# Kernel tuning notes

Measured on AMD Instinct MI355X. Metric: run time of the kernel, lower is better.

Reference implementation:

```python
import jax, jax.numpy as jnp
import numpy as np
from jax import lax

DN = ('NCHW', 'OIHW', 'NCHW')


def conv_reflect(x, w, b, pad):
    # reflect-padded Conv2d (padding_mode='reflect' in torch)
    xp = jnp.pad(x, ((0, 0), (0, 0), (pad, pad), (pad, pad)), mode='reflect')
    y = lax.conv_general_dilated(xp, w, (1, 1), 'VALID', dimension_numbers=DN)
    return y + b[None, :, None, None]


def setup_inputs() -> dict:
    key = jax.random.key(0)
    ks = jax.random.split(key, 11)
    B, C_in, W, H = 2, 20, 1024, 1024
    K = 16          # num_preconv_kernls
    P = 9           # preconv_kernel_size
    hid = 8         # hidden_input_size
    s = 0.05
    x = jax.random.normal(ks[0], (B, C_in, W, H), dtype=jnp.float32)
    w1 = jax.random.normal(ks[1], (16, 20, 7, 7), dtype=jnp.float32) * s
    b1 = jnp.zeros((16,), jnp.float32)
    w2 = jax.random.normal(ks[2], (32, 16, 5, 5), dtype=jnp.float32) * s
    b2 = jnp.zeros((32,), jnp.float32)
    w3 = jax.random.normal(ks[3], (64, 32, 5, 5), dtype=jnp.float32) * s
    b3 = jnp.zeros((64,), jnp.float32)
    w4 = jax.random.normal(ks[4], (hid + K, 64, 5, 5), dtype=jnp.float32) * s
    b4 = jnp.zeros((hid + K,), jnp.float32)
    dwk = (jnp.ones((K, 1, P, P), jnp.float32)
           + jax.random.normal(ks[5], (K, 1, P, P), dtype=jnp.float32) * 0.1) / (P * P)
    return {"x": x, "w1": w1, "b1": b1, "w2": w2, "b2": b2,
            "w3": w3, "b3": b3, "w4": w4, "b4": b4, "dwk": dwk}


def reference(x, w1, b1, w2, b2, w3, b3, w4, b4, dwk):
    B, _, W, H = x.shape
    hid, K, P = 8, 16, 9
    color = x[:, 0:3]                                   # (B,3,W,H)
    h = jax.nn.relu(conv_reflect(x, w1, b1, 3))
    h = jax.nn.relu(conv_reflect(h, w2, b2, 2))
    h = jax.nn.relu(conv_reflect(h, w3, b3, 2))
    raw = conv_reflect(h, w4, b4, 2)                    # (B,24,W,H)
    hidden = raw[:, 0:hid]                              # (B,8,W,H)
    weights = jax.nn.softmax(raw[:, hid:] / 5.0, axis=1)  # (B,16,W,H)
    # depthwise conv of color with 16 kernels per channel (groups=3, zero pad)
    rpk = jnp.tile(dwk, (3, 1, 1, 1))                   # (48,1,P,P)
    pre = lax.conv_general_dilated(color, rpk, (1, 1),
                                   [(P // 2, P // 2), (P // 2, P // 2)],
                                   dimension_numbers=DN,
                                   feature_group_count=3)
    pre = pre.reshape(B, 3, K, W, H)
    filtered = jnp.einsum('bkwh,bckwh->bcwh', weights, pre)
    return jnp.concatenate((filtered, hidden), axis=1)  # (B,11,W,H)
```

## Files before the change

kernel.cpp:

```cpp
#include <hip/hip_runtime.h>

constexpr int IMG = 1024;
constexpr long long HW = (long long)IMG * IMG;

typedef unsigned short u16;
typedef __attribute__((ext_vector_type(8))) short bf16x8;
typedef __attribute__((ext_vector_type(4))) float f32x4;
typedef __attribute__((ext_vector_type(4))) u16 u16x4;

__device__ __forceinline__ int reflect_idx(int i, int n) {
    if (i < 0) i = -i;
    if (i >= n) i = 2 * n - 2 - i;
    return i;
}
__device__ __forceinline__ int iclamp(int v, int lo, int hi) {
    return v < lo ? lo : (v > hi ? hi : v);
}
__device__ __forceinline__ u16 f2bf(float f) {
    unsigned u = __builtin_bit_cast(unsigned, f);
    u += 0x7FFF + ((u >> 16) & 1);
    return (u16)(u >> 16);
}

__global__ void prep_w1(const float* __restrict__ w1, u16* __restrict__ w1p) {
    int i = blockIdx.x * 256 + threadIdx.x;
    if (i >= 49 * 16 * 32) return;
    int tap = i / (16 * 32), rem = i % (16 * 32), co = rem / 32, ci = rem % 32;
    w1p[i] = (ci < 20) ? f2bf(w1[(co * 20 + ci) * 49 + tap]) : (u16)0;
}
__global__ void prep_w2(const float* __restrict__ w2, u16* __restrict__ w2p) {
    int i = blockIdx.x * 256 + threadIdx.x;
    if (i >= 13 * 32 * 32) return;
    int p = i / (32 * 32), rem = i % (32 * 32), co = rem / 32, k = rem % 32;
    int tap = 2 * p + (k >> 4), ci = k & 15;
    w2p[i] = (tap < 25) ? f2bf(w2[(co * 16 + ci) * 25 + tap]) : (u16)0;
}
__global__ void prep_w3(const float* __restrict__ w3, u16* __restrict__ w3p) {
    int i = blockIdx.x * 256 + threadIdx.x;
    if (i >= 25 * 64 * 32) return;
    int tap = i / (64 * 32), rem = i % (64 * 32), co = rem / 32, ci = rem % 32;
    w3p[i] = f2bf(w3[(co * 32 + ci) * 25 + tap]);
}
__global__ void prep_w4(const float* __restrict__ w4, u16* __restrict__ w4p) {
    int i = blockIdx.x * 256 + threadIdx.x;
    if (i >= 25 * 32 * 64) return;
    int tap = i / (32 * 64), rem = i % (32 * 64), co = rem / 64, ci = rem % 64;
    w4p[i] = (co < 24) ? f2bf(w4[(co * 64 + ci) * 25 + tap]) : (u16)0;
}

__global__ __launch_bounds__(256) void conv1_mfma(
    const float* __restrict__ x, const u16* __restrict__ w1p,
    const float* __restrict__ b1, u16* __restrict__ h1,
    int out_base, int out_rows)
{
    constexpr int TS = 22, PAD = 3, UNITS = 4;
    __shared__ u16 tile[TS * TS * 32];

    const int tid = threadIdx.x;
    const int gx0 = blockIdx.x * 16;
    const int gy0 = out_base + blockIdx.y * 16;

    for (int u = tid; u < TS * TS * UNITS; u += 256) {
        int pu = u >> 2, q = u & 3;
        int ty = pu / TS, tx = pu - ty * TS;
        int gy = reflect_idx(gy0 + ty - PAD, IMG);
        int gx = reflect_idx(gx0 + tx - PAD, IMG);
        long long off = (long long)gy * IMG + gx;
        bf16x8 v;
        #pragma unroll
        for (int j = 0; j < 8; ++j) {
            int cc = q * 8 + j;
            float f = (cc < 20) ? x[(long long)cc * HW + off] : 0.f;
            v[j] = (short)f2bf(f);
        }
        *(bf16x8*)&tile[(pu * UNITS + (q ^ (tx & 3))) * 8] = v;
    }
    __syncthreads();

    const int lane = tid & 63, wv = tid >> 6;
    const int l15 = lane & 15, g = lane >> 4;

    f32x4 acc[4];
    #pragma unroll
    for (int y = 0; y < 4; ++y) acc[y] = (f32x4){0.f, 0.f, 0.f, 0.f};

    for (int dx = 0; dx < 7; ++dx) {
        bf16x8 af[7];
        #pragma unroll
        for (int dy = 0; dy < 7; ++dy)
            af[dy] = *(const bf16x8*)&w1p[((dy * 7 + dx) * 16 + l15) * 32 + g * 8];
        bf16x8 bfr[10];
        const int tx = l15 + dx;
        #pragma unroll
        for (int r = 0; r < 10; ++r)
            bfr[r] = *(const bf16x8*)&tile[(((wv * 4 + r) * TS + tx) * UNITS + (g ^ (tx & 3))) * 8];
        #pragma unroll
        for (int yy = 0; yy < 4; ++yy)
            #pragma unroll
            for (int dy = 0; dy < 7; ++dy)
                acc[yy] = __builtin_amdgcn_mfma_f32_16x16x32_bf16(af[dy], bfr[yy + dy], acc[yy], 0, 0, 0);
    }

    const int out_hi = out_base + out_rows;
    float bia[4];
    #pragma unroll
    for (int r = 0; r < 4; ++r) bia[r] = b1[4 * g + r];
    #pragma unroll
    for (int yy = 0; yy < 4; ++yy) {
        int gy = gy0 + wv * 4 + yy;
        if (gy >= out_hi) continue;
        u16x4 pk;
        #pragma unroll
        for (int r = 0; r < 4; ++r)
            pk[r] = f2bf(fmaxf(acc[yy][r] + bia[r], 0.f));
        *(u16x4*)&h1[((long long)(gy - out_base) * IMG + gx0 + l15) * 16 + 4 * g] = pk;
    }
}

__global__ __launch_bounds__(256) void conv2_mfma(
    const u16* __restrict__ h1, const u16* __restrict__ w2p,
    const float* __restrict__ b2, u16* __restrict__ h2,
    int in_base, int in_rows, int out_base, int out_rows)
{
    constexpr int TS = 20, PAD = 2, UNITS = 2;
    __shared__ u16 tile[TS * TS * 16];

    const int tid = threadIdx.x;
    const int gx0 = blockIdx.x * 16;
    const int gy0 = out_base + blockIdx.y * 16;

    for (int u = tid; u < TS * TS * UNITS; u += 256) {
        int pu = u >> 1, q = u & 1;
        int ty = pu / TS, tx = pu - ty * TS;
        int gy = reflect_idx(gy0 + ty - PAD, IMG) - in_base;
        gy = iclamp(gy, 0, in_rows - 1);
        int gx = reflect_idx(gx0 + tx - PAD, IMG);
        bf16x8 v = *(const bf16x8*)&h1[((long long)gy * IMG + gx) * 16 + q * 8];
        *(bf16x8*)&tile[(pu * UNITS + (q ^ (tx & 1))) * 8] = v;
    }
    __syncthreads();

    const int lane = tid & 63, wv = tid >> 6;
    const int l15 = lane & 15, g = lane >> 4;

    f32x4 acc[4][2];
    #pragma unroll
    for (int y = 0; y < 4; ++y) {
        acc[y][0] = (f32x4){0.f, 0.f, 0.f, 0.f};
        acc[y][1] = (f32x4){0.f, 0.f, 0.f, 0.f};
    }

    for (int p = 0; p < 13; ++p) {
        int tap = 2 * p + (g >> 1);
        int tb = tap > 24 ? 24 : tap;
        int dy = tb / 5, dx = tb - dy * 5;
        bf16x8 af0 = *(const bf16x8*)&w2p[(p * 32 + l15) * 32 + g * 8];
        bf16x8 af1 = *(const bf16x8*)&w2p[(p * 32 + 16 + l15) * 32 + g * 8];
        const int tx = l15 + dx;
        #pragma unroll
        for (int yy = 0; yy < 4; ++yy) {
            int ty = wv * 4 + yy + dy;
            bf16x8 bf = *(const bf16x8*)&tile[((ty * TS + tx) * UNITS + ((g & 1) ^ (tx & 1))) * 8];
            acc[yy][0] = __builtin_amdgcn_mfma_f32_16x16x32_bf16(af0, bf, acc[yy][0], 0, 0, 0);
            acc[yy][1] = __builtin_amdgcn_mfma_f32_16x16x32_bf16(af1, bf, acc[yy][1], 0, 0, 0);
        }
    }

    const int out_hi = out_base + out_rows;
    #pragma unroll
    for (int yy = 0; yy < 4; ++yy) {
        int gy = gy0 + wv * 4 + yy;
        if (gy >= out_hi) continue;
        long long pb = ((long long)(gy - out_base) * IMG + gx0 + l15) * 32;
        #pragma unroll
        for (int cb = 0; cb < 2; ++cb) {
            int co = cb * 16 + 4 * g;
            u16x4 pk;
            #pragma unroll
            for (int r = 0; r < 4; ++r)
                pk[r] = f2bf(fmaxf(acc[yy][cb][r] + b2[co + r], 0.f));
            *(u16x4*)&h2[pb + co] = pk;
        }
    }
}

__global__ __launch_bounds__(256) void conv3_mfma(
    const u16* __restrict__ h2, const u16* __restrict__ w3p,
    const float* __restrict__ b3, u16* __restrict__ h3,
    int in_base, int in_rows, int out_base, int out_rows)
{
    constexpr int CI = 32, TS = 20, PAD = 2, UNITS = 4;
    __shared__ u16 tile[TS * TS * CI];

    const int tid = threadIdx.x;
    const int gx0 = blockIdx.x * 16;
    const int gy0 = out_base + blockIdx.y * 16;

    for (int u = tid; u < TS * TS * UNITS; u += 256) {
        int pu = u >> 2, q = u & 3;
        int ty = pu / TS, tx = pu - ty * TS;
        int gy = reflect_idx(gy0 + ty - PAD, IMG) - in_base;
        gy = iclamp(gy, 0, in_rows - 1);
        int gx = reflect_idx(gx0 + tx - PAD, IMG);
        bf16x8 v = *(const bf16x8*)&h2[((long long)gy * IMG + gx) * CI + q * 8];
        *(bf16x8*)&tile[(pu * UNITS + (q ^ (tx & 3))) * 8] = v;
    }
    __syncthreads();

    const int lane = tid & 63, wv = tid >> 6;
    const int l15 = lane & 15, g = lane >> 4;

    f32x4 acc[4][4];
    #pragma unroll
    for (int y = 0; y < 4; ++y)
        #pragma unroll
        for (int cb = 0; cb < 4; ++cb) acc[y][cb] = (f32x4){0.f, 0.f, 0.f, 0.f};

    for (int dx = 0; dx < 5; ++dx) {
        const int tx = l15 + dx;
        const int uu = g ^ (tx & 3);
        bf16x8 bfr[8];
        #pragma unroll
        for (int s = 0; s < 8; ++s)
            bfr[s] = *(const bf16x8*)&tile[(((wv * 4 + s) * TS + tx) * UNITS + uu) * 8];
        #pragma unroll
        for (int dy = 0; dy < 5; ++dy) {
            const int tap = dy * 5 + dx;
            bf16x8 af[4];
            #pragma unroll
            for (int cb = 0; cb < 4; ++cb)
                af[cb] = *(const bf16x8*)&w3p[(tap * 64 + cb * 16 + l15) * 32 + g * 8];
            #pragma unroll
            for (int yy = 0; yy < 4; ++yy)
                #pragma unroll
                for (int cb = 0; cb < 4; ++cb)
                    acc[yy][cb] = __builtin_amdgcn_mfma_f32_16x16x32_bf16(af[cb], bfr[yy + dy], acc[yy][cb], 0, 0, 0);
        }
    }

    const int out_hi = out_base + out_rows;
    #pragma unroll
    for (int yy = 0; yy < 4; ++yy) {
        int gy = gy0 + wv * 4 + yy;
        if (gy >= out_hi) continue;
        long long pb = ((long long)(gy - out_base) * IMG + gx0 + l15) * 64;
        #pragma unroll
        for (int cb = 0; cb < 4; ++cb) {
            int co = cb * 16 + 4 * g;
            u16x4 pk;
            #pragma unroll
            for (int r = 0; r < 4; ++r)
                pk[r] = f2bf(fmaxf(acc[yy][cb][r] + b3[co + r], 0.f));
            *(u16x4*)&h3[pb + co] = pk;
        }
    }
}

__global__ __launch_bounds__(256) void conv4_mfma(
    const u16* __restrict__ h3, const u16* __restrict__ w4p,
    const float* __restrict__ b4, float* __restrict__ out,
    float* __restrict__ wsoft, int in_base, int in_rows, int row0, int nrows)
{
    constexpr int CI = 64, TS = 20, PAD = 2, UNITS = 4;
    __shared__ u16 tile[TS * TS * 32];

    const int tid = threadIdx.x;
    const int gx0 = blockIdx.x * 16;
    const int gy0 = row0 + blockIdx.y * 16;

    const int lane = tid & 63, wv = tid >> 6;
    const int l15 = lane & 15, g = lane >> 4;

    f32x4 acc[4][2];
    #pragma unroll
    for (int y = 0; y < 4; ++y) {
        acc[y][0] = (f32x4){0.f, 0.f, 0.f, 0.f};
        acc[y][1] = (f32x4){0.f, 0.f, 0.f, 0.f};
    }

    #pragma unroll
    for (int half = 0; half < 2; ++half) {
        if (half) __syncthreads();
        for (int u = tid; u < TS * TS * UNITS; u += 256) {
            int pu = u >> 2, q = u & 3;
            int ty = pu / TS, tx = pu - ty * TS;
            int gy = reflect_idx(gy0 + ty - PAD, IMG) - in_base;
            gy = iclamp(gy, 0, in_rows - 1);
            int gx = reflect_idx(gx0 + tx - PAD, IMG);
            bf16x8 v = *(const bf16x8*)&h3[((long long)gy * IMG + gx) * CI + half * 32 + q * 8];
            *(bf16x8*)&tile[(pu * UNITS + (q ^ (tx & 3))) * 8] = v;
        }
        __syncthreads();

        for (int dx = 0; dx < 5; ++dx) {
            const int tx = l15 + dx;
            const int uu = g ^ (tx & 3);
            bf16x8 bfr[8];
            #pragma unroll
            for (int s = 0; s < 8; ++s)
                bfr[s] = *(const bf16x8*)&tile[(((wv * 4 + s) * TS + tx) * UNITS + uu) * 8];
            #pragma unroll
            for (int dy = 0; dy < 5; ++dy) {
                const int tap = dy * 5 + dx;
                bf16x8 af0 = *(const bf16x8*)&w4p[(tap * 32 + l15) * 64 + half * 32 + g * 8];
                bf16x8 af1 = *(const bf16x8*)&w4p[(tap * 32 + 16 + l15) * 64 + half * 32 + g * 8];
                #pragma unroll
                for (int yy = 0; yy < 4; ++yy) {
                    acc[yy][0] = __builtin_amdgcn_mfma_f32_16x16x32_bf16(af0, bfr[yy + dy], acc[yy][0], 0, 0, 0);
                    acc[yy][1] = __builtin_amdgcn_mfma_f32_16x16x32_bf16(af1, bfr[yy + dy], acc[yy][1], 0, 0, 0);
                }
            }
        }
    }

    float bia0[4], bia1[4];
    #pragma unroll
    for (int r = 0; r < 4; ++r) {
        bia0[r] = b4[4 * g + r];
        int c1 = 16 + 4 * g + r;
        bia1[r] = (c1 < 24) ? b4[c1] : 0.f;
    }

    #pragma unroll
    for (int yy = 0; yy < 4; ++yy) {
        int gy = gy0 + wv * 4 + yy;
        long long pg = (long long)gy * IMG + gx0 + l15;
        float v0[4], v1[4];
        #pragma unroll
        for (int r = 0; r < 4; ++r) {
            v0[r] = acc[yy][0][r] + bia0[r];
            v1[r] = acc[yy][1][r] + bia1[r];
        }
        if (g < 2) {
            #pragma unroll
            for (int r = 0; r < 4; ++r)
                out[(long long)(3 + 4 * g + r) * HW + pg] = v0[r];
        }
        float s[4];
        int kbase;
        if (g < 2) {
            kbase = 8 + 4 * g;
            #pragma unroll
            for (int r = 0; r < 4; ++r) s[r] = v1[r] * 0.2f;
        } else {
            kbase = 4 * (g - 2);
            #pragma unroll
            for (int r = 0; r < 4; ++r) s[r] = v0[r] * 0.2f;
        }
        float m = fmaxf(fmaxf(s[0], s[1]), fmaxf(s[2], s[3]));
        m = fmaxf(m, __shfl_xor(m, 16));
        m = fmaxf(m, __shfl_xor(m, 32));
        float e[4], loc = 0.f;
        #pragma unroll
        for (int r = 0; r < 4; ++r) { e[r] = __expf(s[r] - m); loc += e[r]; }
        loc += __shfl_xor(loc, 16);
        loc += __shfl_xor(loc, 32);
        float inv = 1.f / loc;
        long long pl = (long long)(gy - row0) * IMG + gx0 + l15;
        #pragma unroll
        for (int r = 0; r < 4; ++r)
            wsoft[(long long)(kbase + r) * nrows * IMG + pl] = e[r] * inv;
    }
}

__global__ __launch_bounds__(256) void apply_filter(
    const float* __restrict__ x, const float* __restrict__ dwk,
    const float* __restrict__ wsoft, float* __restrict__ out,
    int row0, int nrows)
{
    constexpr int PAD = 4, TSF = 40;
    __shared__ float ctile[3][TSF * TSF];

    const int tid = threadIdx.x;
    const int tx = tid & 7, ty = tid >> 3;
    const int bx = blockIdx.x * 32;
    const int gy0 = row0 + blockIdx.y * 32;

    for (int c = 0; c < 3; ++c)
        for (int idx = tid; idx < TSF * TSF; idx += 256) {
            int ly = idx / TSF, lx = idx - ly * TSF;
            int gy = gy0 + ly - PAD, gx = bx + lx - PAD;
            float v = 0.f;
            if (gy >= 0 && gy < IMG && gx >= 0 && gx < IMG)
                v = x[(long long)c * HW + (long long)gy * IMG + gx];
            ctile[c][idx] = v;
        }
    __syncthreads();

    const int gy = gy0 + ty;
    const int xq = bx + tx * 4;

    float wreg[16][4];
    #pragma unroll
    for (int k = 0; k < 16; ++k) {
        f32x4 wv4 = *(const f32x4*)&wsoft[((long long)k * nrows + (gy - row0)) * IMG + xq];
        #pragma unroll
        for (int p = 0; p < 4; ++p) wreg[k][p] = wv4[p];
    }

    float f[3][4];
    #pragma unroll
    for (int c = 0; c < 3; ++c)
        #pragma unroll
        for (int p = 0; p < 4; ++p) f[c][p] = 0.f;

    for (int dy = 0; dy < 9; ++dy) {
        float c9[9][4];
        #pragma unroll
        for (int dxx = 0; dxx < 9; ++dxx)
            #pragma unroll
            for (int p = 0; p < 4; ++p) c9[dxx][p] = 0.f;
        #pragma unroll
        for (int k = 0; k < 16; ++k) {
            #pragma unroll
            for (int dxx = 0; dxx < 9; ++dxx) {
                float s = dwk[k * 81 + dy * 9 + dxx];
                #pragma unroll
                for (int p = 0; p < 4; ++p) c9[dxx][p] += s * wreg[k][p];
            }
        }
        #pragma unroll
        for (int c = 0; c < 3; ++c) {
            const float* crow = &ctile[c][(ty + dy) * TSF + tx * 4];
            f32x4 q0 = *(const f32x4*)crow;
            f32x4 q1 = *(const f32x4*)(crow + 4);
            f32x4 q2 = *(const f32x4*)(crow + 8);
            float win[12];
            #pragma unroll
            for (int j = 0; j < 4; ++j) { win[j] = q0[j]; win[4 + j] = q1[j]; win[8 + j] = q2[j]; }
            #pragma unroll
            for (int dxx = 0; dxx < 9; ++dxx)
                #pragma unroll
                for (int p = 0; p < 4; ++p)
                    f[c][p] += c9[dxx][p] * win[dxx + p];
        }
    }

    #pragma unroll
    for (int c = 0; c < 3; ++c) {
        f32x4 o = { f[c][0], f[c][1], f[c][2], f[c][3] };
        *(f32x4*)&out[(long long)c * HW + (long long)gy * IMG + xq] = o;
    }
}

static inline int hmax(int a, int b) { return a > b ? a : b; }
static inline int hmin(int a, int b) { return a < b ? a : b; }

extern "C" void kernel_launch(void* const* d_in, const int* in_sizes, int n_in,
                              void* d_out, int out_size, void* d_ws, size_t ws_size,
                              hipStream_t stream) {
    const float* x   = (const float*)d_in[0];
    const float* w1  = (const float*)d_in[1];
    const float* b1  = (const float*)d_in[2];
    const float* w2  = (const float*)d_in[3];
    const float* b2  = (const float*)d_in[4];
    const float* w3  = (const float*)d_in[5];
    const float* b3  = (const float*)d_in[6];
    const float* w4  = (const float*)d_in[7];
    const float* b4  = (const float*)d_in[8];
    const float* dwk = (const float*)d_in[9];
    float* out = (float*)d_out;

    int R = 32;
    const int cand[6] = {1024, 512, 256, 128, 64, 32};
    for (int i = 0; i < 6; ++i) {
        long long r = cand[i];
        size_t need = 32768ULL * (r + 12) + 65536ULL * (r + 8)
                    + 131072ULL * (r + 4) + 65536ULL * r + 400000ULL;
        if (need <= ws_size) { R = cand[i]; break; }
    }

    u16*   h1    = (u16*)d_ws;
    u16*   h2    = h1 + (long long)(R + 12) * IMG * 16;
    u16*   h3    = h2 + (long long)(R + 8) * IMG * 32;
    float* wsoft = (float*)(h3 + (long long)(R + 4) * IMG * 64);
    u16*   w1p   = (u16*)(wsoft + 16LL * R * IMG);
    u16*   w2p   = w1p + 49 * 16 * 32;
    u16*   w3p   = w2p + 13 * 32 * 32;
    u16*   w4p   = w3p + 25 * 64 * 32;

    dim3 blk(256);
    prep_w1<<<dim3(98),  blk, 0, stream>>>(w1, w1p);
    prep_w2<<<dim3(52),  blk, 0, stream>>>(w2, w2p);
    prep_w3<<<dim3(200), blk, 0, stream>>>(w3, w3p);
    prep_w4<<<dim3(200), blk, 0, stream>>>(w4, w4p);

    const int nstripes = IMG / R;
    for (int b = 0; b < 2; ++b) {
        const float* x_b = x + (long long)b * 20 * HW;
        float* out_b = out + (long long)b * 11 * HW;
        for (int s = 0; s < nstripes; ++s) {
            const int r0 = s * R;
            const int h1_lo = hmax(0, r0 - 6), h1_hi = hmin(IMG, r0 + R + 6), h1_r = h1_hi - h1_lo;
            const int h2_lo = hmax(0, r0 - 4), h2_hi = hmin(IMG, r0 + R + 4), h2_r = h2_hi - h2_lo;
            const int h3_lo = hmax(0, r0 - 2), h3_hi = hmin(IMG, r0 + R + 2), h3_r = h3_hi - h3_lo;

            conv1_mfma<<<dim3(64, (h1_r + 15) / 16, 1), blk, 0, stream>>>(
                x_b, w1p, b1, h1, h1_lo, h1_r);
            conv2_mfma<<<dim3(64, (h2_r + 15) / 16, 1), blk, 0, stream>>>(
                h1, w2p, b2, h2, h1_lo, h1_r, h2_lo, h2_r);
            conv3_mfma<<<dim3(64, (h3_r + 15) / 16, 1), blk, 0, stream>>>(
                h2, w3p, b3, h3, h2_lo, h2_r, h3_lo, h3_r);
            conv4_mfma<<<dim3(64, R / 16, 1), blk, 0, stream>>>(
                h3, w4p, b4, out_b, wsoft, h3_lo, h3_r, r0, R);
            apply_filter<<<dim3(32, R / 32, 1), blk, 0, stream>>>(
                x_b, dwk, wsoft, out_b, r0, R);
        }
    }
}
```

Baseline: 1.204 ms.

## Stage conv3/conv4 input tiles via direct global-to-LDS loads and double-buffer conv4 halves

Replaces register-staged tile fills in conv3 and conv4 with __builtin_amdgcn_global_load_lds direct-to-LDS 16-byte loads. The swizzle moves from the LDS destination to the global source address, because each wave writes a contiguous 1 KiB LDS chunk. conv4 now uses two LDS tiles and issues the second-half load before computing on the first, so the load can overlap with MFMA work. This doubles conv4's LDS footprint, which may lower occupancy. Correctness depends on the direct-LDS load semantics and on the __syncthreads placement making the data visible.

```diff
diff --git a/kernel.cpp b/kernel.cpp
--- a/kernel.cpp
+++ b/kernel.cpp
@@ -195,20 +195,22 @@
     const int tid = threadIdx.x;
     const int gx0 = blockIdx.x * 16;
     const int gy0 = out_base + blockIdx.y * 16;
-
-    for (int u = tid; u < TS * TS * UNITS; u += 256) {
-        int pu = u >> 2, q = u & 3;
-        int ty = pu / TS, tx = pu - ty * TS;
-        int gy = reflect_idx(gy0 + ty - PAD, IMG) - in_base;
-        gy = iclamp(gy, 0, in_rows - 1);
-        int gx = reflect_idx(gx0 + tx - PAD, IMG);
-        bf16x8 v = *(const bf16x8*)&h2[((long long)gy * IMG + gx) * CI + q * 8];
-        *(bf16x8*)&tile[(pu * UNITS + (q ^ (tx & 3))) * 8] = v;
-    }
-    __syncthreads();
-
     const int lane = tid & 63, wv = tid >> 6;
     const int l15 = lane & 15, g = lane >> 4;
+
+    for (int gidx = wv; gidx < 25; gidx += 4) {
+        int j = (gidx << 6) + lane;
+        int pu = j >> 2, qq = j & 3;
+        int ty = pu / TS, tx = pu - ty * TS;
+        int gy = iclamp(reflect_idx(gy0 + ty - PAD, IMG) - in_base, 0, in_rows - 1);
+        int gx = reflect_idx(gx0 + tx - PAD, IMG);
+        const u16* src = &h2[((long long)gy * IMG + gx) * CI + ((qq ^ (tx & 3)) << 3)];
+        __builtin_amdgcn_global_load_lds(
+            (const __attribute__((address_space(1))) void*)src,
+            (__attribute__((address_space(3))) void*)&tile[(long long)gidx << 9],
+            16, 0, 0);
+    }
+    __syncthreads();
 
     f32x4 acc[4][4];
     #pragma unroll
@@ -262,14 +264,29 @@
     float* __restrict__ wsoft, int in_base, int in_rows, int row0, int nrows)
 {
     constexpr int CI = 64, TS = 20, PAD = 2, UNITS = 4;
-    __shared__ u16 tile[TS * TS * 32];
+    __shared__ u16 tileA[TS * TS * 32];
+    __shared__ u16 tileB[TS * TS * 32];
 
     const int tid = threadIdx.x;
     const int gx0 = blockIdx.x * 16;
     const int gy0 = row0 + blockIdx.y * 16;
-
     const int lane = tid & 63, wv = tid >> 6;
     const int l15 = lane & 15, g = lane >> 4;
+
+    auto STAGE = [&](u16* tl, int half) {
+        for (int gidx = wv; gidx < 25; gidx += 4) {
+            int j = (gidx << 6) + lane;
+            int pu = j >> 2, qq = j & 3;
+            int ty = pu / TS, tx = pu - ty * TS;
+            int gy = iclamp(reflect_idx(gy0 + ty - PAD, IMG) - in_base, 0, in_rows - 1);
+            int gx = reflect_idx(gx0 + tx - PAD, IMG);
+            const u16* src = &h3[((long long)gy * IMG + gx) * CI + half * 32 + ((qq ^ (tx & 3)) << 3)];
+            __builtin_amdgcn_global_load_lds(
+                (const __attribute__((address_space(1))) void*)src,
+                (__attribute__((address_space(3))) void*)&tl[(long long)gidx << 9],
+                16, 0, 0);
+        }
+    };
 
     f32x4 acc[4][2];
     #pragma unroll
@@ -278,27 +295,21 @@
         acc[y][1] = (f32x4){0.f, 0.f, 0.f, 0.f};
     }
 
+    STAGE(tileA, 0);
+    __syncthreads();
+    STAGE(tileB, 1);
+
     #pragma unroll
     for (int half = 0; half < 2; ++half) {
+        const u16* tl = half ? tileB : tileA;
         if (half) __syncthreads();
-        for (int u = tid; u < TS * TS * UNITS; u += 256) {
-            int pu = u >> 2, q = u & 3;
-            int ty = pu / TS, tx = pu - ty * TS;
-            int gy = reflect_idx(gy0 + ty - PAD, IMG) - in_base;
-            gy = iclamp(gy, 0, in_rows - 1);
-            int gx = reflect_idx(gx0 + tx - PAD, IMG);
-            bf16x8 v = *(const bf16x8*)&h3[((long long)gy * IMG + gx) * CI + half * 32 + q * 8];
-            *(bf16x8*)&tile[(pu * UNITS + (q ^ (tx & 3))) * 8] = v;
-        }
-        __syncthreads();
-
         for (int dx = 0; dx < 5; ++dx) {
             const int tx = l15 + dx;
             const int uu = g ^ (tx & 3);
             bf16x8 bfr[8];
             #pragma unroll
             for (int s = 0; s < 8; ++s)
-                bfr[s] = *(const bf16x8*)&tile[(((wv * 4 + s) * TS + tx) * UNITS + uu) * 8];
+                bfr[s] = *(const bf16x8*)&tl[(((wv * 4 + s) * TS + tx) * UNITS + uu) * 8];
             #pragma unroll
             for (int dy = 0; dy < 5; ++dy) {
                 const int tap = dy * 5 + dx;
```

New measurement: 1.155 ms. -4.0%, faster.
